# Optimization experiments

Hardware: AMD Instinct MI355X
Metric: run time of the kernel (lower is better)

The kernel has to match this reference:

```python
import jax, jax.numpy as jnp
import numpy as np
import math

B, A, D = 32, 100, 10000
HID = 256
NH = 4
OUT = 10000
NFREQ = 16
E = round(OUT * 0.5 / (A / 2))  # max_entries = 100
N = int(math.sqrt(D))           # 100 (row/col decode of flat index)
SCALE = math.sqrt(HID)
STEPS = 3


def swish(x):
    return x * jax.nn.sigmoid(x)


def setup_inputs() -> dict:
    key = jax.random.key(0)
    ks = jax.random.split(key, 16)
    s = 0.02
    p = lambda k, shape: jax.random.normal(k, shape, jnp.float32) * s
    vals = jax.random.normal(ks[0], (B, A, D), jnp.float32)
    keep = jax.random.uniform(ks[1], (B, A, D)) < (E / D)  # ~E nonzeros per (b, agent)
    x = vals * keep
    return {
        "x": x,
        "fourier_B": jax.random.normal(ks[2], (NFREQ, 2), jnp.float32),
        "enc_W1": p(ks[3], (HID, 1 + 2 * NFREQ)), "enc_b1": jnp.zeros((HID,), jnp.float32),
        "enc_W2": p(ks[4], (HID, HID)), "enc_b2": jnp.zeros((HID,), jnp.float32),
        "pad_token": jnp.zeros((HID,), jnp.float32),
        "comp_W1": p(ks[5], (2 * HID, E * HID)), "comp_b1": jnp.zeros((2 * HID,), jnp.float32),
        "comp_W2": p(ks[6], (HID, 2 * HID)), "comp_b2": jnp.zeros((HID,), jnp.float32),
        "connectivity": jax.random.normal(ks[7], (A, A), jnp.float32),
        "qW": p(ks[8], (NH, HID, HID)), "kW": p(ks[9], (NH, HID, HID)), "vW": p(ks[10], (NH, HID, HID)),
        "fp_W1": p(ks[11], (NH, HID, HID)), "fp_b1": jnp.zeros((NH, HID), jnp.float32),
        "fp_W2": p(ks[12], (NH, HID, HID)), "fp_b2": jnp.zeros((NH, HID), jnp.float32),
        "ln_g": jnp.ones((NH, HID), jnp.float32), "ln_b": jnp.zeros((NH, HID), jnp.float32),
        "out_W": p(ks[13], (OUT, HID)), "out_b": jnp.zeros((OUT,), jnp.float32),
    }


def reference(x, fourier_B, enc_W1, enc_b1, enc_W2, enc_b2, pad_token,
              comp_W1, comp_b1, comp_W2, comp_b2, connectivity,
              qW, kW, vW, fp_W1, fp_b1, fp_W2, fp_b2, ln_g, ln_b, out_W, out_b):
    # --- ragged gather of nonzero entries, truncated/padded to E per (b, agent) ---
    mask = x != 0                                                   # [B,A,D]
    # stable argsort puts nonzero positions first, in ascending flat-index order
    # (same order as torch .nonzero per batch row)
    idx = jnp.argsort(jnp.logical_not(mask), axis=-1, stable=True)[..., :E]  # [B,A,E]
    valid = jnp.take_along_axis(mask, idx, axis=-1)                 # [B,A,E]
    vals = jnp.take_along_axis(x, idx, axis=-1)[..., None]          # [B,A,E,1]
    coords = jnp.stack([idx // N, idx % N], axis=-1).astype(x.dtype)  # [B,A,E,2]
    # Fourier positional encoding
    proj = (2.0 * math.pi) * jnp.einsum('baec,fc->baef', coords, fourier_B)
    pos = jnp.concatenate([jnp.sin(proj), jnp.cos(proj)], axis=-1)  # [B,A,E,2F]
    feat = jnp.concatenate([vals, pos], axis=-1)                    # [B,A,E,1+2F]
    # entry encoder MLP
    e = swish(feat @ enc_W1.T + enc_b1) @ enc_W2.T + enc_b2         # [B,A,E,HID]
    e = jnp.where(valid[..., None], e, pad_token)                   # pad slots -> pad_token
    # per-agent compression of the E entry embeddings
    flat = e.reshape(B, A, E * HID)
    h = swish(flat @ comp_W1.T + comp_b1) @ comp_W2.T + comp_b2     # [B,A,HID]

    # --- message passing: multi-head dot-product GAT with learned connectivity bias ---
    conn = connectivity[None, None]                                  # broadcast [1,1,A,A]
    for _ in range(STEPS):
        Q = jnp.einsum('bai,nji->nbaj', h, qW)                      # [NH,B,A,HID]
        K = jnp.einsum('bai,nji->nbaj', h, kW)
        V = jnp.einsum('bai,nji->nbaj', h, vW)
        scores = jnp.einsum('nbaj,nbcj->nbac', Q, K) / SCALE + conn
        alpha = jax.nn.softmax(scores, axis=-1)                     # dropout p=0.0
        Hm = jnp.einsum('nbac,nbcj->nbaj', alpha, V)
        t = jnp.einsum('nbaj,nij->nbai', swish(Hm), fp_W1) + fp_b1[:, None, None, :]
        t = jnp.einsum('nbaj,nij->nbai', swish(t), fp_W2) + fp_b2[:, None, None, :]
        m = t.mean(-1, keepdims=True)
        v = ((t - m) ** 2).mean(-1, keepdims=True)
        o = (t - m) / jnp.sqrt(v + 1e-5) * ln_g[:, None, None, :] + ln_b[:, None, None, :]
        h = o.mean(0)                                               # mean over heads

    return h @ out_W.T + out_b                                      # [B,A,OUT]
```

## Files before the change

### kernel.cpp

```cpp
#include <hip/hip_runtime.h>
#include <cstdint>
#include <cstddef>

#define NBATCH 32
#define NAGENT 100
#define NDIM   10000
#define HID    256
#define NHEAD  4
#define NOUT   10000
#define NFREQ  16
#define EMAX   100
#define NBA    3200
#define KBIG   25600
#define TWO_PI 6.283185307179586476925f

typedef float  v4f  __attribute__((ext_vector_type(4)));
typedef short  v8s  __attribute__((ext_vector_type(8)));

__device__ __forceinline__ unsigned short bf_hi(float f) {
    unsigned int u = __float_as_uint(f);
    return (unsigned short)((u + 0x7FFFu + ((u >> 16) & 1u)) >> 16);
}
__device__ __forceinline__ float bf_tof(unsigned short h) {
    return __uint_as_float(((unsigned int)h) << 16);
}

__device__ __forceinline__ void gld16(const void* g, void* l) {
    __builtin_amdgcn_global_load_lds(
        (const __attribute__((address_space(1))) void*)g,
        (__attribute__((address_space(3))) void*)l, 16, 0, 0);
}

__global__ __launch_bounds__(64) void k_extract(const float* __restrict__ x,
                                                int* __restrict__ idxb,
                                                float* __restrict__ valb,
                                                int* __restrict__ nvalid)
{
    const int ba = blockIdx.x;
    const float* xr = x + (size_t)ba * NDIM;
    const int lane = threadIdx.x;
    int base = 0;
    for (int c0 = 0; c0 < NDIM; c0 += 64) {
        int i = c0 + lane;
        float v = (i < NDIM) ? xr[i] : 0.0f;
        unsigned long long m = __ballot(v != 0.0f);
        if (v != 0.0f) {
            int p = base + __popcll(m & ((1ull << lane) - 1ull));
            if (p < EMAX) {
                idxb[(size_t)ba * EMAX + p] = i;
                valb[(size_t)ba * EMAX + p] = v;
            }
        }
        base += __popcll(m);
        if (base >= EMAX) break;
    }
    if (lane == 0) nvalid[ba] = base < EMAX ? base : EMAX;
}

__global__ __launch_bounds__(256) void k_g1(
    const int* __restrict__ idxb, const float* __restrict__ valb,
    const int* __restrict__ nvalid, const float* __restrict__ fourB,
    const float* __restrict__ W1, const float* __restrict__ b1,
    unsigned short* __restrict__ g1h, unsigned short* __restrict__ g1l)
{
    __shared__ float s_feat[16][36];
    __shared__ float s_w[8448];
    __shared__ float s_b1v[256];
    __shared__ int   s_idx[16];
    __shared__ int   s_valid[16];

    const int t  = threadIdx.x;
    const int g0 = blockIdx.x * 16;

    if (t < 16) {
        int g = g0 + t;
        int ba = g / 100, slot = g - ba * 100;
        int valid = (slot < nvalid[ba]) ? 1 : 0;
        s_valid[t]   = valid;
        s_idx[t]     = valid ? idxb[g] : 0;
        s_feat[t][0] = valid ? valb[g] : 0.0f;
    }
    s_b1v[t] = b1[t];
    for (int i = t; i < 8448; i += 256) s_w[i] = W1[i];
    __syncthreads();

    {
        int ent = t >> 4, f = t & 15;
        float sv = 0.0f, cv = 0.0f;
        if (s_valid[ent]) {
            int id = s_idx[ent];
            float row = (float)(id / 100);
            float col = (float)(id % 100);
            float pr = TWO_PI * (row * fourB[2 * f] + col * fourB[2 * f + 1]);
            sv = sinf(pr); cv = cosf(pr);
        }
        s_feat[ent][1 + f]  = sv;
        s_feat[ent][17 + f] = cv;
    }
    __syncthreads();

    const float* wr = &s_w[t * 33];
    for (int ent = 0; ent < 16; ++ent) {
        float a = s_b1v[t];
        #pragma unroll
        for (int c = 0; c < 33; ++c) a += s_feat[ent][c] * wr[c];
        float g = a / (1.0f + expf(-a));
        g = s_valid[ent] ? g : 0.0f;
        unsigned short h = bf_hi(g);
        unsigned short l = bf_hi(g - bf_tof(h));
        size_t o = (size_t)(g0 + ent) * 256 + t;
        g1h[o] = h;
        g1l[o] = l;
    }
}

__global__ void k_w2t(const float* __restrict__ W2, float* __restrict__ W2T)
{
    int kp = blockIdx.x, k = threadIdx.x;
    W2T[kp * 256 + k] = W2[k * 256 + kp];
}

__global__ __launch_bounds__(256) void k_wsplit(const float* __restrict__ src,
                                                unsigned short* __restrict__ hi,
                                                unsigned short* __restrict__ lo)
{
    int i = (blockIdx.x * 256 + threadIdx.x) * 4;
    float4 f = *(const float4*)(src + i);
    ushort4 h, l;
    h.x = bf_hi(f.x); l.x = bf_hi(f.x - bf_tof(h.x));
    h.y = bf_hi(f.y); l.y = bf_hi(f.y - bf_tof(h.y));
    h.z = bf_hi(f.z); l.z = bf_hi(f.z - bf_tof(h.z));
    h.w = bf_hi(f.w); l.w = bf_hi(f.w - bf_tof(h.w));
    *(ushort4*)(hi + i) = h;
    *(ushort4*)(lo + i) = l;
}

__global__ __launch_bounds__(256) void k_tables(
    const float* __restrict__ W1, const float* __restrict__ pad,
    const float* __restrict__ b2, float* __restrict__ D, float* __restrict__ E0)
{
    __shared__ float red[4];
    const int n = blockIdx.x;
    const int t = threadIdx.x, lane = t & 63, w = t >> 6;
    const float pm = pad[t] - b2[t];
    const float bb = b2[t];
    const float* wr = W1 + (size_t)n * KBIG;
    float eb = 0.0f;
    for (int s = 0; s < 100; ++s) {
        float wv = wr[s * 256 + t];
        float p = pm * wv;
        eb += bb * wv;
        #pragma unroll
        for (int o = 32; o > 0; o >>= 1) p += __shfl_down(p, o);
        if (lane == 0) red[w] = p;
        __syncthreads();
        if (t == 0) D[s * 512 + n] = red[0] + red[1] + red[2] + red[3];
        __syncthreads();
    }
    #pragma unroll
    for (int o = 32; o > 0; o >>= 1) eb += __shfl_down(eb, o);
    if (lane == 0) red[w] = eb;
    __syncthreads();
    if (t == 0) E0[n] = red[0] + red[1] + red[2] + red[3];
}

__global__ void k_suffix(const float* __restrict__ D, float* __restrict__ Corr)
{
    int n = blockIdx.x * 256 + threadIdx.x;
    float c = 0.0f;
    Corr[100 * 512 + n] = 0.0f;
    for (int s = 99; s >= 0; --s) { c += D[s * 512 + n]; Corr[s * 512 + n] = c; }
}

template<int ACT, int SPLIT>
__global__ __launch_bounds__(256) void k_gemmbf(
    const unsigned short* __restrict__ Ah, const unsigned short* __restrict__ Al,
    const unsigned short* __restrict__ Wh, const unsigned short* __restrict__ Wl,
    const float* __restrict__ bias, float* __restrict__ C,
    unsigned short* __restrict__ Ch, unsigned short* __restrict__ Cl,
    int M, int N, int K,
    long long sA, long long sW, long long sBias, long long sC)
{
    __shared__ unsigned short lds[2][4][4096];
    const int t = threadIdx.x;
    const int z = blockIdx.z;
    Ah += (size_t)z * sA;  Al += (size_t)z * sA;
    Wh += (size_t)z * sW;  Wl += (size_t)z * sW;
    if (SPLIT) { Ch += (size_t)z * sC; Cl += (size_t)z * sC; }
    else       { C  += (size_t)z * sC; }
    const float* bp = bias ? (bias + (size_t)z * sBias) : nullptr;
    const int bn = blockIdx.x * 128, bm = blockIdx.y * 128;
    const int lane = t & 63, w = t >> 6;
    const int wm = (w & 1) * 64, wn = (w >> 1) * 64;

    const int sr = w * 16 + (lane >> 2);
    const int so = (lane & 3) * 8;
    int rw0 = bn + sr;       if (rw0 >= N) rw0 = N - 1;
    int rw1 = bn + 64 + sr;  if (rw1 >= N) rw1 = N - 1;
    const unsigned short* gA0 = Ah + (size_t)(bm + sr) * K + so;
    const unsigned short* gA1 = Ah + (size_t)(bm + 64 + sr) * K + so;
    const unsigned short* ga0 = Al + (size_t)(bm + sr) * K + so;
    const unsigned short* ga1 = Al + (size_t)(bm + 64 + sr) * K + so;
    const unsigned short* gW0 = Wh + (size_t)rw0 * K + so;
    const unsigned short* gW1 = Wh + (size_t)rw1 * K + so;
    const unsigned short* gw0 = Wl + (size_t)rw0 * K + so;
    const unsigned short* gw1 = Wl + (size_t)rw1 * K + so;
    const int lb0 = w * 512;
    const int lb1 = 2048 + w * 512;

    v4f acc[4][4] = {};
    const int fr = lane & 15, fq = (lane >> 4) * 8;
    const int KT = K >> 5;

#define STAGE_G(buf, o)                                                        \
    gld16(gA0 + (o), &lds[buf][0][lb0]); gld16(gA1 + (o), &lds[buf][0][lb1]);  \
    gld16(ga0 + (o), &lds[buf][1][lb0]); gld16(ga1 + (o), &lds[buf][1][lb1]);  \
    gld16(gW0 + (o), &lds[buf][2][lb0]); gld16(gW1 + (o), &lds[buf][2][lb1]);  \
    gld16(gw0 + (o), &lds[buf][3][lb0]); gld16(gw1 + (o), &lds[buf][3][lb1]);

    STAGE_G(0, 0);
    __syncthreads();
    int cur = 0;
    for (int kt = 0; kt < KT; ++kt) {
        if (kt + 1 < KT) { STAGE_G(cur ^ 1, (kt + 1) * 32); }
        v8s ahf[4], alf[4], bhf[4], blf[4];
        #pragma unroll
        for (int i = 0; i < 4; ++i) {
            ahf[i] = *(const v8s*)&lds[cur][0][(wm + i * 16 + fr) * 32 + fq];
            alf[i] = *(const v8s*)&lds[cur][1][(wm + i * 16 + fr) * 32 + fq];
            bhf[i] = *(const v8s*)&lds[cur][2][(wn + i * 16 + fr) * 32 + fq];
            blf[i] = *(const v8s*)&lds[cur][3][(wn + i * 16 + fr) * 32 + fq];
        }
        #pragma unroll
        for (int mi = 0; mi < 4; ++mi)
            #pragma unroll
            for (int ni = 0; ni < 4; ++ni) {
                acc[mi][ni] = __builtin_amdgcn_mfma_f32_16x16x32_bf16(ahf[mi], bhf[ni], acc[mi][ni], 0, 0, 0);
                acc[mi][ni] = __builtin_amdgcn_mfma_f32_16x16x32_bf16(ahf[mi], blf[ni], acc[mi][ni], 0, 0, 0);
                acc[mi][ni] = __builtin_amdgcn_mfma_f32_16x16x32_bf16(alf[mi], bhf[ni], acc[mi][ni], 0, 0, 0);
            }
        __syncthreads();
        cur ^= 1;
    }
#undef STAGE_G

    const int er = (lane >> 4) * 4, ec = lane & 15;
    #pragma unroll
    for (int mi = 0; mi < 4; ++mi)
        #pragma unroll
        for (int ni = 0; ni < 4; ++ni) {
            int m = bm + wm + mi * 16 + er;
            int n = bn + wn + ni * 16 + ec;
            if (n < N) {
                float bv = bp ? bp[n] : 0.0f;
                #pragma unroll
                for (int r = 0; r < 4; ++r) {
                    float val = acc[mi][ni][r] + bv;
                    if (ACT == 1) val = val / (1.0f + expf(-val));
                    if (SPLIT) {
                        unsigned short hv = bf_hi(val);
                        Ch[(size_t)(m + r) * N + n] = hv;
                        Cl[(size_t)(m + r) * N + n] = bf_hi(val - bf_tof(hv));
                    } else {
                        C[(size_t)(m + r) * N + n] = val;
                    }
                }
            }
        }
    (void)M;
}

__global__ __launch_bounds__(256) void k_g3mfma(
    const unsigned short* __restrict__ Ah, const unsigned short* __restrict__ Al,
    const unsigned short* __restrict__ Wh, const unsigned short* __restrict__ Wl,
    float* __restrict__ part)
{
    __shared__ unsigned short lds[2][4][4096];
    const int t  = threadIdx.x;
    const int hwid = blockIdx.x;
    const int wk = (hwid & 7) * 100 + (hwid >> 3);
    const int bn = (wk & 3) * 128;
    const int bm = ((wk >> 2) % 25) * 128;
    const int z  = wk / 100;
    const int lane = t & 63, w = t >> 6;
    const int wm = (w & 1) * 64, wn = (w >> 1) * 64;
    const size_t K = KBIG;

    const int sr = w * 16 + (lane >> 2);
    const int so = (lane & 3) * 8;
    const size_t zo = (size_t)z * 3200 + so;
    const unsigned short* gA0 = Ah + (size_t)(bm + sr) * K + zo;
    const unsigned short* gA1 = Ah + (size_t)(bm + 64 + sr) * K + zo;
    const unsigned short* ga0 = Al + (size_t)(bm + sr) * K + zo;
    const unsigned short* ga1 = Al + (size_t)(bm + 64 + sr) * K + zo;
    const unsigned short* gW0 = Wh + (size_t)(bn + sr) * K + zo;
    const unsigned short* gW1 = Wh + (size_t)(bn + 64 + sr) * K + zo;
    const unsigned short* gw0 = Wl + (size_t)(bn + sr) * K + zo;
    const unsigned short* gw1 = Wl + (size_t)(bn + 64 + sr) * K + zo;
    const int lb0 = w * 512, lb1 = 2048 + w * 512;

    v4f acc[4][4] = {};
    const int fr = lane & 15, fq = (lane >> 4) * 8;

#define STAGE_Z(buf, o)                                                        \
    gld16(gA0 + (o), &lds[buf][0][lb0]); gld16(gA1 + (o), &lds[buf][0][lb1]);  \
    gld16(ga0 + (o), &lds[buf][1][lb0]); gld16(ga1 + (o), &lds[buf][1][lb1]);  \
    gld16(gW0 + (o), &lds[buf][2][lb0]); gld16(gW1 + (o), &lds[buf][2][lb1]);  \
    gld16(gw0 + (o), &lds[buf][3][lb0]); gld16(gw1 + (o), &lds[buf][3][lb1]);

    STAGE_Z(0, 0);
    __syncthreads();
    int cur = 0;
    for (int kt = 0; kt < 100; ++kt) {
        if (kt < 99) { STAGE_Z(cur ^ 1, (kt + 1) * 32); }
        v8s ah[4], al[4], bh[4], bl[4];
        #pragma unroll
        for (int i = 0; i < 4; ++i) {
            ah[i] = *(const v8s*)&lds[cur][0][(wm + i * 16 + fr) * 32 + fq];
            al[i] = *(const v8s*)&lds[cur][1][(wm + i * 16 + fr) * 32 + fq];
            bh[i] = *(const v8s*)&lds[cur][2][(wn + i * 16 + fr) * 32 + fq];
            bl[i] = *(const v8s*)&lds[cur][3][(wn + i * 16 + fr) * 32 + fq];
        }
        #pragma unroll
        for (int mi = 0; mi < 4; ++mi)
            #pragma unroll
            for (int ni = 0; ni < 4; ++ni) {
                acc[mi][ni] = __builtin_amdgcn_mfma_f32_16x16x32_bf16(ah[mi], bh[ni], acc[mi][ni], 0, 0, 0);
                acc[mi][ni] = __builtin_amdgcn_mfma_f32_16x16x32_bf16(ah[mi], bl[ni], acc[mi][ni], 0, 0, 0);
                acc[mi][ni] = __builtin_amdgcn_mfma_f32_16x16x32_bf16(al[mi], bh[ni], acc[mi][ni], 0, 0, 0);
            }
        __syncthreads();
        cur ^= 1;
    }
#undef STAGE_Z

    const int er = (lane >> 4) * 4, ec = lane & 15;
    float* cp = part + (size_t)z * NBA * 512;
    #pragma unroll
    for (int mi = 0; mi < 4; ++mi)
        #pragma unroll
        for (int ni = 0; ni < 4; ++ni) {
            int m = bm + wm + mi * 16 + er;
            int n = bn + wn + ni * 16 + ec;
            #pragma unroll
            for (int r = 0; r < 4; ++r)
                cp[(size_t)(m + r) * 512 + n] = acc[mi][ni][r];
        }
}

__global__ __launch_bounds__(256) void k_g3red(
    const float* __restrict__ part, const float* __restrict__ comp_b1,
    const float* __restrict__ E0, const float* __restrict__ Corr,
    const int* __restrict__ nvalid,
    unsigned short* __restrict__ oh, unsigned short* __restrict__ ol)
{
    const int i4 = (blockIdx.x * 256 + threadIdx.x) * 4;
    const int ba = i4 >> 9, n = i4 & 511;
    const size_t S = (size_t)NBA * 512;
    float4 s = *(const float4*)(part + i4);
    #pragma unroll
    for (int zz = 1; zz < 8; ++zz) {
        float4 p = *(const float4*)(part + zz * S + i4);
        s.x += p.x; s.y += p.y; s.z += p.z; s.w += p.w;
    }
    int nv = nvalid[ba];
    float4 b  = *(const float4*)(comp_b1 + n);
    float4 e  = *(const float4*)(E0 + n);
    float4 c  = *(const float4*)(Corr + nv * 512 + n);
    float r0 = s.x + b.x + e.x + c.x;
    float r1 = s.y + b.y + e.y + c.y;
    float r2 = s.z + b.z + e.z + c.z;
    float r3 = s.w + b.w + e.w + c.w;
    float4 o;
    o.x = r0 / (1.0f + expf(-r0));
    o.y = r1 / (1.0f + expf(-r1));
    o.z = r2 / (1.0f + expf(-r2));
    o.w = r3 / (1.0f + expf(-r3));
    ushort4 h, l;
    h.x = bf_hi(o.x); l.x = bf_hi(o.x - bf_tof(h.x));
    h.y = bf_hi(o.y); l.y = bf_hi(o.y - bf_tof(h.y));
    h.z = bf_hi(o.z); l.z = bf_hi(o.z - bf_tof(h.z));
    h.w = bf_hi(o.w); l.w = bf_hi(o.w - bf_tof(h.w));
    *(ushort4*)(oh + i4) = h;
    *(ushort4*)(ol + i4) = l;
}

__global__ __launch_bounds__(256) void k_attn(
    const float* __restrict__ Qb, const float* __restrict__ Kb,
    const float* __restrict__ Vb, const float* __restrict__ conn,
    unsigned short* __restrict__ Oh, unsigned short* __restrict__ Ol)
{
    __shared__ float sKV[256][101];
    __shared__ float sAl[50][100];
    __shared__ float sQ[2][256];
    __shared__ float sRed[2][2];

    const int t = threadIdx.x;
    const int half = blockIdx.x, b = blockIdx.y, n = blockIdx.z;
    const size_t base = ((size_t)n * NBA + b * 100) * 256;

    const float* Kp = Kb + base;
    for (int r = 0; r < 100; ++r) sKV[t][r] = Kp[(size_t)r * 256 + t];
    __syncthreads();

    const float* Qp = Qb + base;
    const int pair = t >> 7, tt = t & 127, lane = t & 63, wvi = t >> 6;

    for (int rr = 0; rr < 25; ++rr) {
        const int row0 = half * 50 + rr * 2;
        const int lr = rr * 2 + pair;
        __syncthreads();
        sQ[0][t] = Qp[(size_t)(row0)*256 + t];
        sQ[1][t] = Qp[(size_t)(row0 + 1) * 256 + t];
        __syncthreads();
        float sc = 0.0f;
        if (tt < 100) {
            const float* qr = sQ[pair];
            float p0 = 0.f, p1 = 0.f, p2 = 0.f, p3 = 0.f;
            #pragma unroll 4
            for (int c = 0; c < 256; c += 4) {
                p0 += qr[c]     * sKV[c][tt];
                p1 += qr[c + 1] * sKV[c + 1][tt];
                p2 += qr[c + 2] * sKV[c + 2][tt];
                p3 += qr[c + 3] * sKV[c + 3][tt];
            }
            sc = ((p0 + p1) + (p2 + p3)) * 0.0625f + conn[(row0 + pair) * 100 + tt];
            sAl[lr][tt] = sc;
        }
        __syncthreads();
        if ((wvi & 1) == 0) {
            int p = wvi >> 1;
            int r2 = rr * 2 + p;
            float m = sAl[r2][lane];
            if (lane < 36) m = fmaxf(m, sAl[r2][lane + 64]);
            #pragma unroll
            for (int off = 32; off > 0; off >>= 1)
                m = fmaxf(m, __shfl_down(m, off));
            if (lane == 0) sRed[0][p] = m;
        }
        __syncthreads();
        float ex = 0.0f;
        if (tt < 100) {
            ex = expf(sc - sRed[0][pair]);
            sAl[lr][tt] = ex;
        }
        __syncthreads();
        if ((wvi & 1) == 0) {
            int p = wvi >> 1;
            int r2 = rr * 2 + p;
            float s = sAl[r2][lane];
            if (lane < 36) s += sAl[r2][lane + 64];
            #pragma unroll
            for (int off = 32; off > 0; off >>= 1)
                s += __shfl_down(s, off);
            if (lane == 0) sRed[1][p] = s;
        }
        __syncthreads();
        if (tt < 100) sAl[lr][tt] = ex / sRed[1][pair];
    }
    __syncthreads();

    const float* Vp = Vb + base;
    for (int r = 0; r < 100; ++r) sKV[t][r] = Vp[(size_t)r * 256 + t];
    __syncthreads();

    for (int rr = 0; rr < 50; ++rr) {
        int row = half * 50 + rr;
        float a = 0.0f;
        #pragma unroll 4
        for (int j = 0; j < 100; ++j) a += sAl[rr][j] * sKV[t][j];
        float sw = a / (1.0f + expf(-a));
        size_t oidx = base + (size_t)row * 256 + t;
        unsigned short hv = bf_hi(sw);
        Oh[oidx] = hv;
        Ol[oidx] = bf_hi(sw - bf_tof(hv));
    }
}

__global__ __launch_bounds__(256) void k_ln_mean(
    const float* __restrict__ t2b, const float* __restrict__ ln_g,
    const float* __restrict__ ln_b,
    unsigned short* __restrict__ hh, unsigned short* __restrict__ hl)
{
    __shared__ float so[4][256];
    const int ba = blockIdx.x, t = threadIdx.x;
    const int n = t >> 6, lane = t & 63;
    const float* tr = t2b + ((size_t)n * NBA + ba) * HID;
    float4 v = *(const float4*)(tr + lane * 4);
    float s1 = v.x + v.y + v.z + v.w;
    float s2 = v.x * v.x + v.y * v.y + v.z * v.z + v.w * v.w;
    #pragma unroll
    for (int off = 32; off > 0; off >>= 1) {
        s1 += __shfl_down(s1, off);
        s2 += __shfl_down(s2, off);
    }
    s1 = __shfl(s1, 0);
    s2 = __shfl(s2, 0);
    float m = s1 * (1.0f / 256.0f);
    float var = s2 * (1.0f / 256.0f) - m * m;
    float rstd = 1.0f / sqrtf(var + 1e-5f);
    float4 gv = *(const float4*)(ln_g + n * HID + lane * 4);
    float4 bv = *(const float4*)(ln_b + n * HID + lane * 4);
    float4 o;
    o.x = (v.x - m) * rstd * gv.x + bv.x;
    o.y = (v.y - m) * rstd * gv.y + bv.y;
    o.z = (v.z - m) * rstd * gv.z + bv.z;
    o.w = (v.w - m) * rstd * gv.w + bv.w;
    *(float4*)&so[n][lane * 4] = o;
    __syncthreads();
    float hv = 0.25f * (so[0][t] + so[1][t] + so[2][t] + so[3][t]);
    unsigned short hi = bf_hi(hv);
    size_t oidx = (size_t)ba * HID + t;
    hh[oidx] = hi;
    hl[oidx] = bf_hi(hv - bf_tof(hi));
}

extern "C" void kernel_launch(void* const* d_in, const int* in_sizes, int n_in,
                              void* d_out, int out_size, void* d_ws, size_t ws_size,
                              hipStream_t stream)
{
    const float* x       = (const float*)d_in[0];
    const float* fourB   = (const float*)d_in[1];
    const float* enc_W1  = (const float*)d_in[2];
    const float* enc_b1  = (const float*)d_in[3];
    const float* enc_W2  = (const float*)d_in[4];
    const float* enc_b2  = (const float*)d_in[5];
    const float* pad_tok = (const float*)d_in[6];
    const float* comp_W1 = (const float*)d_in[7];
    const float* comp_b1 = (const float*)d_in[8];
    const float* comp_W2 = (const float*)d_in[9];
    const float* comp_b2 = (const float*)d_in[10];
    const float* conn    = (const float*)d_in[11];
    const float* qW      = (const float*)d_in[12];
    const float* kW      = (const float*)d_in[13];
    const float* vW      = (const float*)d_in[14];
    const float* fpW1    = (const float*)d_in[15];
    const float* fpb1    = (const float*)d_in[16];
    const float* fpW2    = (const float*)d_in[17];
    const float* fpb2    = (const float*)d_in[18];
    const float* ln_g    = (const float*)d_in[19];
    const float* ln_b    = (const float*)d_in[20];
    const float* out_W   = (const float*)d_in[21];
    const float* out_b   = (const float*)d_in[22];
    float* outp = (float*)d_out;

    char* ws = (char*)d_ws;
    size_t off = 0;
    auto alloc = [&](size_t bytes) -> void* {
        void* p = (void*)(ws + off);
        off += (bytes + 255) & ~(size_t)255;
        return p;
    };
    int*   idxb = (int*)  alloc((size_t)NBA * EMAX * 4);
    float* valb = (float*)alloc((size_t)NBA * EMAX * 4);
    int*   nval = (int*)  alloc((size_t)NBA * 4);
    unsigned short* g1h = (unsigned short*)alloc((size_t)NBA * KBIG * 2);
    unsigned short* g1l = (unsigned short*)alloc((size_t)NBA * KBIG * 2);
    float* W2T  = (float*)alloc((size_t)256 * 256 * 4);
    float* W1p  = (float*)alloc((size_t)512 * KBIG * 4);
    float* part = W1p;
    unsigned short* Whi = (unsigned short*)alloc((size_t)512 * KBIG * 2);
    unsigned short* Wlo = (unsigned short*)alloc((size_t)512 * KBIG * 2);
    float* Dt   = (float*)alloc((size_t)100 * 512 * 4);
    float* Corr = (float*)alloc((size_t)101 * 512 * 4);
    float* E0   = (float*)alloc((size_t)512 * 4);
    float* Qb   = (float*)alloc((size_t)NHEAD * NBA * HID * 4);
    float* Kb   = (float*)alloc((size_t)NHEAD * NBA * HID * 4);
    float* Vb   = (float*)alloc((size_t)NHEAD * NBA * HID * 4);
    unsigned short* asplh = (unsigned short*)alloc((size_t)NHEAD * NBA * HID * 2);
    unsigned short* aspll = (unsigned short*)alloc((size_t)NHEAD * NBA * HID * 2);
    unsigned short* cW1h = (unsigned short*)Qb;
    unsigned short* cW1l = (unsigned short*)Vb;
    unsigned short* bsplh = g1h;
    unsigned short* bspll = g1h + (size_t)NHEAD * NBA * HID;
    unsigned short* w2tH = (unsigned short*)alloc((size_t)256 * 256 * 2);
    unsigned short* w2tL = (unsigned short*)alloc((size_t)256 * 256 * 2);
    unsigned short* qkvWh = (unsigned short*)alloc((size_t)3 * NHEAD * HID * HID * 2);
    unsigned short* qkvWl = (unsigned short*)alloc((size_t)3 * NHEAD * HID * HID * 2);
    unsigned short* f1Wh = (unsigned short*)alloc((size_t)NHEAD * HID * HID * 2);
    unsigned short* f1Wl = (unsigned short*)alloc((size_t)NHEAD * HID * HID * 2);
    unsigned short* f2Wh = (unsigned short*)alloc((size_t)NHEAD * HID * HID * 2);
    unsigned short* f2Wl = (unsigned short*)alloc((size_t)NHEAD * HID * HID * 2);
    unsigned short* c2Wh = (unsigned short*)alloc((size_t)HID * 512 * 2);
    unsigned short* c2Wl = (unsigned short*)alloc((size_t)HID * 512 * 2);
    unsigned short* oWh  = (unsigned short*)alloc((size_t)NOUT * HID * 2);
    unsigned short* oWl  = (unsigned short*)alloc((size_t)NOUT * HID * 2);
    float* t2b  = Vb;

    const long long sW = (long long)HID * HID;
    const long long sC = (long long)NBA * HID;

    k_extract<<<NBA, 64, 0, stream>>>(x, idxb, valb, nval);
    k_g1<<<NBA * EMAX / 16, 256, 0, stream>>>(idxb, valb, nval, fourB,
                                              enc_W1, enc_b1, g1h, g1l);

    k_w2t<<<256, 256, 0, stream>>>(enc_W2, W2T);
    k_wsplit<<<256 * 256 / 1024, 256, 0, stream>>>(W2T, w2tH, w2tL);
    k_wsplit<<<512 * KBIG / 1024, 256, 0, stream>>>(comp_W1, cW1h, cW1l);
    k_gemmbf<0, 0><<<dim3(2, 400, 1), 256, 0, stream>>>(
        cW1h, cW1l, w2tH, w2tL, nullptr, W1p, nullptr, nullptr,
        512 * EMAX, 256, 256, 0, 0, 0, 0);
    k_wsplit<<<512 * KBIG / 1024, 256, 0, stream>>>(W1p, Whi, Wlo);
    k_tables<<<512, 256, 0, stream>>>(comp_W1, pad_tok, enc_b2, Dt, E0);
    k_suffix<<<2, 256, 0, stream>>>(Dt, Corr);

    k_wsplit<<<NHEAD * 65536 / 1024, 256, 0, stream>>>(qW, qkvWh, qkvWl);
    k_wsplit<<<NHEAD * 65536 / 1024, 256, 0, stream>>>(kW, qkvWh + NHEAD * 65536, qkvWl + NHEAD * 65536);
    k_wsplit<<<NHEAD * 65536 / 1024, 256, 0, stream>>>(vW, qkvWh + 2 * NHEAD * 65536, qkvWl + 2 * NHEAD * 65536);
    k_wsplit<<<NHEAD * 65536 / 1024, 256, 0, stream>>>(fpW1, f1Wh, f1Wl);
    k_wsplit<<<NHEAD * 65536 / 1024, 256, 0, stream>>>(fpW2, f2Wh, f2Wl);
    k_wsplit<<<HID * 512 / 1024, 256, 0, stream>>>(comp_W2, c2Wh, c2Wl);
    k_wsplit<<<NOUT * HID / 1024, 256, 0, stream>>>(out_W, oWh, oWl);

    k_g3mfma<<<800, 256, 0, stream>>>(g1h, g1l, Whi, Wlo, part);
    k_g3red<<<NBA * 512 / 1024, 256, 0, stream>>>(part, comp_b1, E0, Corr, nval, asplh, aspll);
    k_gemmbf<0, 1><<<dim3(2, 25, 1), 256, 0, stream>>>(
        asplh, aspll, c2Wh, c2Wl, comp_b2, nullptr, bsplh, bspll,
        NBA, HID, 512, 0, 0, 0, 0);

    for (int step = 0; step < 3; ++step) {
        k_gemmbf<0, 0><<<dim3(2, 25, 12), 256, 0, stream>>>(
            bsplh, bspll, qkvWh, qkvWl, nullptr, Qb, nullptr, nullptr,
            NBA, HID, HID, 0, sW, 0, sC);
        k_attn<<<dim3(2, NBATCH, NHEAD), 256, 0, stream>>>(Qb, Kb, Vb, conn, asplh, aspll);
        k_gemmbf<1, 1><<<dim3(2, 25, 4), 256, 0, stream>>>(
            asplh, aspll, f1Wh, f1Wl, fpb1, nullptr, bsplh, bspll,
            NBA, HID, HID, sC, sW, HID, sC);
        k_gemmbf<0, 0><<<dim3(2, 25, 4), 256, 0, stream>>>(
            bsplh, bspll, f2Wh, f2Wl, fpb2, t2b, nullptr, nullptr,
            NBA, HID, HID, sC, sW, HID, sC);
        k_ln_mean<<<NBA, 256, 0, stream>>>(t2b, ln_g, ln_b, bsplh, bspll);
    }

    k_gemmbf<0, 0><<<dim3(79, 25, 1), 256, 0, stream>>>(
        bsplh, bspll, oWh, oWl, out_b, outp, nullptr, nullptr,
        NBA, NOUT, HID, 0, 0, 0, 0);

    (void)in_sizes; (void)n_in; (void)out_size; (void)ws_size;
}
```

Measured before the change: 1.825 ms.

## Fuse weight splits, drop fp32 intermediates, and tighten encoder and table kernels

Measured after the change: 1.793 ms. Within noise of the previous version (-1.8%).

```diff
diff --git a/kernel.cpp b/kernel.cpp
--- a/kernel.cpp
+++ b/kernel.cpp
@@ -65,7 +65,6 @@
 {
     __shared__ float s_feat[16][36];
     __shared__ float s_w[8448];
-    __shared__ float s_b1v[256];
     __shared__ int   s_idx[16];
     __shared__ int   s_valid[16];
 
@@ -80,8 +79,8 @@
         s_idx[t]     = valid ? idxb[g] : 0;
         s_feat[t][0] = valid ? valb[g] : 0.0f;
     }
-    s_b1v[t] = b1[t];
     for (int i = t; i < 8448; i += 256) s_w[i] = W1[i];
+    const float b1t = b1[t];
     __syncthreads();
 
     {
@@ -99,11 +98,20 @@
     }
     __syncthreads();
 
-    const float* wr = &s_w[t * 33];
+    float wreg[33];
+    #pragma unroll
+    for (int c = 0; c < 33; ++c) wreg[c] = s_w[t * 33 + c];
+
     for (int ent = 0; ent < 16; ++ent) {
-        float a = s_b1v[t];
-        #pragma unroll
-        for (int c = 0; c < 33; ++c) a += s_feat[ent][c] * wr[c];
+        const float* fr_ = &s_feat[ent][0];
+        float a = b1t;
+        #pragma unroll
+        for (int c4 = 0; c4 < 8; ++c4) {
+            float4 f = *(const float4*)(fr_ + c4 * 4);
+            a += f.x * wreg[c4 * 4] + f.y * wreg[c4 * 4 + 1]
+               + f.z * wreg[c4 * 4 + 2] + f.w * wreg[c4 * 4 + 3];
+        }
+        a += fr_[32] * wreg[32];
         float g = a / (1.0f + expf(-a));
         g = s_valid[ent] ? g : 0.0f;
         unsigned short h = bf_hi(g);
@@ -114,10 +122,15 @@
     }
 }
 
-__global__ void k_w2t(const float* __restrict__ W2, float* __restrict__ W2T)
+__global__ void k_w2t(const float* __restrict__ W2,
+                      unsigned short* __restrict__ w2tH,
+                      unsigned short* __restrict__ w2tL)
 {
     int kp = blockIdx.x, k = threadIdx.x;
-    W2T[kp * 256 + k] = W2[k * 256 + kp];
+    float v = W2[k * 256 + kp];
+    unsigned short h = bf_hi(v);
+    w2tH[kp * 256 + k] = h;
+    w2tL[kp * 256 + k] = bf_hi(v - bf_tof(h));
 }
 
 __global__ __launch_bounds__(256) void k_wsplit(const float* __restrict__ src,
@@ -135,6 +148,37 @@
     *(ushort4*)(lo + i) = l;
 }
 
+__global__ __launch_bounds__(256) void k_wsplit_all(
+    const float* __restrict__ qW, const float* __restrict__ kW,
+    const float* __restrict__ vW, const float* __restrict__ fpW1,
+    const float* __restrict__ fpW2, const float* __restrict__ comp_W2,
+    const float* __restrict__ out_W,
+    unsigned short* __restrict__ qkvWh, unsigned short* __restrict__ qkvWl,
+    unsigned short* __restrict__ f1Wh, unsigned short* __restrict__ f1Wl,
+    unsigned short* __restrict__ f2Wh, unsigned short* __restrict__ f2Wl,
+    unsigned short* __restrict__ c2Wh, unsigned short* __restrict__ c2Wl,
+    unsigned short* __restrict__ oWh, unsigned short* __restrict__ oWl)
+{
+    const int b = blockIdx.x;
+    const float* src; unsigned short* hi; unsigned short* lo; int rel;
+    if (b < 256)        { src = qW;      hi = qkvWh;          lo = qkvWl;          rel = b; }
+    else if (b < 512)   { src = kW;      hi = qkvWh + 262144; lo = qkvWl + 262144; rel = b - 256; }
+    else if (b < 768)   { src = vW;      hi = qkvWh + 524288; lo = qkvWl + 524288; rel = b - 512; }
+    else if (b < 1024)  { src = fpW1;    hi = f1Wh;           lo = f1Wl;           rel = b - 768; }
+    else if (b < 1280)  { src = fpW2;    hi = f2Wh;           lo = f2Wl;           rel = b - 1024; }
+    else if (b < 1408)  { src = comp_W2; hi = c2Wh;           lo = c2Wl;           rel = b - 1280; }
+    else                { src = out_W;   hi = oWh;            lo = oWl;            rel = b - 1408; }
+    int i = (rel * 256 + threadIdx.x) * 4;
+    float4 f = *(const float4*)(src + i);
+    ushort4 h, l;
+    h.x = bf_hi(f.x); l.x = bf_hi(f.x - bf_tof(h.x));
+    h.y = bf_hi(f.y); l.y = bf_hi(f.y - bf_tof(h.y));
+    h.z = bf_hi(f.z); l.z = bf_hi(f.z - bf_tof(h.z));
+    h.w = bf_hi(f.w); l.w = bf_hi(f.w - bf_tof(h.w));
+    *(ushort4*)(hi + i) = h;
+    *(ushort4*)(lo + i) = l;
+}
+
 __global__ __launch_bounds__(256) void k_tables(
     const float* __restrict__ W1, const float* __restrict__ pad,
     const float* __restrict__ b2, float* __restrict__ D, float* __restrict__ E0)
@@ -142,20 +186,18 @@
     __shared__ float red[4];
     const int n = blockIdx.x;
     const int t = threadIdx.x, lane = t & 63, w = t >> 6;
-    const float pm = pad[t] - b2[t];
-    const float bb = b2[t];
+    float4 pd = *(const float4*)(pad + lane * 4);
+    float4 b4 = *(const float4*)(b2 + lane * 4);
+    float4 pm4 = make_float4(pd.x - b4.x, pd.y - b4.y, pd.z - b4.z, pd.w - b4.w);
     const float* wr = W1 + (size_t)n * KBIG;
     float eb = 0.0f;
-    for (int s = 0; s < 100; ++s) {
-        float wv = wr[s * 256 + t];
-        float p = pm * wv;
-        eb += bb * wv;
+    for (int s = w; s < 100; s += 4) {
+        float4 wv = *(const float4*)(wr + s * 256 + lane * 4);
+        float p = pm4.x * wv.x + pm4.y * wv.y + pm4.z * wv.z + pm4.w * wv.w;
+        eb += b4.x * wv.x + b4.y * wv.y + b4.z * wv.z + b4.w * wv.w;
         #pragma unroll
         for (int o = 32; o > 0; o >>= 1) p += __shfl_down(p, o);
-        if (lane == 0) red[w] = p;
-        __syncthreads();
-        if (t == 0) D[s * 512 + n] = red[0] + red[1] + red[2] + red[3];
-        __syncthreads();
+        if (lane == 0) D[s * 512 + n] = p;
     }
     #pragma unroll
     for (int o = 32; o > 0; o >>= 1) eb += __shfl_down(eb, o);
@@ -556,9 +598,6 @@
     int*   nval = (int*)  alloc((size_t)NBA * 4);
     unsigned short* g1h = (unsigned short*)alloc((size_t)NBA * KBIG * 2);
     unsigned short* g1l = (unsigned short*)alloc((size_t)NBA * KBIG * 2);
-    float* W2T  = (float*)alloc((size_t)256 * 256 * 4);
-    float* W1p  = (float*)alloc((size_t)512 * KBIG * 4);
-    float* part = W1p;
     unsigned short* Whi = (unsigned short*)alloc((size_t)512 * KBIG * 2);
     unsigned short* Wlo = (unsigned short*)alloc((size_t)512 * KBIG * 2);
     float* Dt   = (float*)alloc((size_t)100 * 512 * 4);
@@ -571,8 +610,11 @@
     unsigned short* aspll = (unsigned short*)alloc((size_t)NHEAD * NBA * HID * 2);
     unsigned short* cW1h = (unsigned short*)Qb;
     unsigned short* cW1l = (unsigned short*)Vb;
-    unsigned short* bsplh = g1h;
-    unsigned short* bspll = g1h + (size_t)NHEAD * NBA * HID;
+    float* part = Qb;
+    unsigned short* h1sh  = g1h;
+    unsigned short* h1sl  = g1h + (size_t)NBA * 512;
+    unsigned short* bsplh = g1h + (size_t)2 * NBA * 512;
+    unsigned short* bspll = bsplh + (size_t)NHEAD * NBA * HID;
     unsigned short* w2tH = (unsigned short*)alloc((size_t)256 * 256 * 2);
     unsigned short* w2tL = (unsigned short*)alloc((size_t)256 * 256 * 2);
     unsigned short* qkvWh = (unsigned short*)alloc((size_t)3 * NHEAD * HID * HID * 2);
@@ -594,28 +636,22 @@
     k_g1<<<NBA * EMAX / 16, 256, 0, stream>>>(idxb, valb, nval, fourB,
                                               enc_W1, enc_b1, g1h, g1l);
 
-    k_w2t<<<256, 256, 0, stream>>>(enc_W2, W2T);
-    k_wsplit<<<256 * 256 / 1024, 256, 0, stream>>>(W2T, w2tH, w2tL);
+    k_w2t<<<256, 256, 0, stream>>>(enc_W2, w2tH, w2tL);
     k_wsplit<<<512 * KBIG / 1024, 256, 0, stream>>>(comp_W1, cW1h, cW1l);
-    k_gemmbf<0, 0><<<dim3(2, 400, 1), 256, 0, stream>>>(
-        cW1h, cW1l, w2tH, w2tL, nullptr, W1p, nullptr, nullptr,
+    k_gemmbf<0, 1><<<dim3(2, 400, 1), 256, 0, stream>>>(
+        cW1h, cW1l, w2tH, w2tL, nullptr, nullptr, Whi, Wlo,
         512 * EMAX, 256, 256, 0, 0, 0, 0);
-    k_wsplit<<<512 * KBIG / 1024, 256, 0, stream>>>(W1p, Whi, Wlo);
     k_tables<<<512, 256, 0, stream>>>(comp_W1, pad_tok, enc_b2, Dt, E0);
     k_suffix<<<2, 256, 0, stream>>>(Dt, Corr);
 
-    k_wsplit<<<NHEAD * 65536 / 1024, 256, 0, stream>>>(qW, qkvWh, qkvWl);
-    k_wsplit<<<NHEAD * 65536 / 1024, 256, 0, stream>>>(kW, qkvWh + NHEAD * 65536, qkvWl + NHEAD * 65536);
-    k_wsplit<<<NHEAD * 65536 / 1024, 256, 0, stream>>>(vW, qkvWh + 2 * NHEAD * 65536, qkvWl + 2 * NHEAD * 65536);
-    k_wsplit<<<NHEAD * 65536 / 1024, 256, 0, stream>>>(fpW1, f1Wh, f1Wl);
-    k_wsplit<<<NHEAD * 65536 / 1024, 256, 0, stream>>>(fpW2, f2Wh, f2Wl);
-    k_wsplit<<<HID * 512 / 1024, 256, 0, stream>>>(comp_W2, c2Wh, c2Wl);
-    k_wsplit<<<NOUT * HID / 1024, 256, 0, stream>>>(out_W, oWh, oWl);
+    k_wsplit_all<<<3908, 256, 0, stream>>>(
+        qW, kW, vW, fpW1, fpW2, comp_W2, out_W,
+        qkvWh, qkvWl, f1Wh, f1Wl, f2Wh, f2Wl, c2Wh, c2Wl, oWh, oWl);
 
     k_g3mfma<<<800, 256, 0, stream>>>(g1h, g1l, Whi, Wlo, part);
-    k_g3red<<<NBA * 512 / 1024, 256, 0, stream>>>(part, comp_b1, E0, Corr, nval, asplh, aspll);
+    k_g3red<<<NBA * 512 / 1024, 256, 0, stream>>>(part, comp_b1, E0, Corr, nval, h1sh, h1sl);
     k_gemmbf<0, 1><<<dim3(2, 25, 1), 256, 0, stream>>>(
-        asplh, aspll, c2Wh, c2Wl, comp_b2, nullptr, bsplh, bspll,
+        h1sh, h1sl, c2Wh, c2Wl, comp_b2, nullptr, bsplh, bspll,
         NBA, HID, 512, 0, 0, 0, 0);
 
     for (int step = 0; step < 3; ++step) {
```
